# Optimization experiments

Measured on AMD Instinct MI355X. Metric: run time of the kernel, lower is better.

The kernel has to match this reference:

```python
import jax, jax.numpy as jnp
import numpy as np

NCH, P, T, BS = 129, 4, 64000, 8
FRM_RATE, TC, HAIR_TC, SHFT, FAC = 16, 8.0, 0.5, 0, 1.0
L_FRM = FRM_RATE * (2 ** (4 + SHFT))            # 256 samples per frame
ALPHA = float(np.exp(-1.0 / (TC * 2 ** (4 + SHFT))))       # temporal integrator pole
BETA = float(np.exp(-1.0 / (HAIR_TC * 2 ** (4 + SHFT))))   # hair-cell LPF pole


def setup_inputs() -> dict:
    rng = np.random.default_rng(0)
    # stable order-4 cochlear IIRs: 2 conjugate pole pairs inside unit circle
    r = rng.uniform(0.8, 0.97, (NCH, P // 2))
    th = rng.uniform(0.05, np.pi - 0.05, (NCH, P // 2))
    A = np.stack([
        np.poly(np.concatenate([r[c] * np.exp(1j * th[c]), r[c] * np.exp(-1j * th[c])])).real
        for c in range(NCH)
    ]).astype(np.float32)                        # [NCH, P+1], A[:,0]==1
    B = (rng.standard_normal((NCH, P + 1)) * 0.1).astype(np.float32)
    key = jax.random.key(0)
    wav = jax.random.normal(key, (BS, T), dtype=jnp.float32)
    return {"wavData": wav, "coch_B": jnp.asarray(B), "coch_A": jnp.asarray(A)}


def iir_lfilter(b, a, x):
    # b, a: [nCh, P+1] (a[:,0] == 1), x: [bs, T] -> y: [nCh, bs, T]
    # direct-form II transposed, all channels in one scan over time
    bt = b[:, None, :]                           # [nCh, 1, P+1]
    at = a[:, None, :]
    z0 = jnp.zeros((b.shape[0], x.shape[0], b.shape[1] - 1), x.dtype)

    def step(z, xt):                             # z: [nCh, bs, P], xt: [bs]
        y = bt[..., 0] * xt[None, :] + z[..., 0]
        z_shift = jnp.concatenate([z[..., 1:], jnp.zeros_like(z[..., :1])], -1)
        z = z_shift + bt[..., 1:] * xt[None, :, None] - at[..., 1:] * y[..., None]
        return z, y

    _, y = jax.lax.scan(step, z0, x.T)           # y: [T, nCh, bs]
    return jnp.moveaxis(y, 0, -1)                # [nCh, bs, T]


def first_order_iir(x, c):
    # y[t] = x[t] + c * y[t-1] along the last axis (lfilter b=[1,0], a=[1,-c])
    def combine(e1, e2):
        a1, b1 = e1
        a2, b2 = e2
        return a1 * a2, b1 * a2 + b2

    coef = jnp.full_like(x, jnp.asarray(c, x.dtype))
    _, y = jax.lax.associative_scan(combine, (coef, x), axis=-1)
    return y


def reference(wavData, coch_B, coch_A):
    y1 = iir_lfilter(coch_B, coch_A, wavData)        # cochlear filterbank [nCh, bs, T]
    y2 = jax.nn.sigmoid(FAC * y1)                    # hair-cell nonlinearity
    y2 = first_order_iir(y2, BETA)                   # hair-cell membrane LPF
    y2_prev = jnp.concatenate([y2[:1], y2[:-1]], 0)  # previous channel (ch 0 diffs itself -> 0)
    y4 = jnp.maximum(y2 - y2_prev, 0.0)              # lateral inhibition + half-wave rectify
    y5 = first_order_iir(y4, ALPHA)                  # temporal integration (alpha != 0 branch)
    aud = y5[..., 0:T - 1:L_FRM]                     # frame-rate downsample [nCh, bs, nFrm]
    return jnp.transpose(aud, (1, 0, 2))             # [bs, nCh, nFrm]
```

## Files before the change

### kernel.cpp

```cpp
#include <hip/hip_runtime.h>
#include <math.h>

#define NCH 129
#define BS 8
#define TLEN 64000
#define TILE 256
#define WARM 64
#define ZLEAD 256
#define NFRM 250
#define NSEQ (NCH * BS)
#define NBK (BS * NFRM)
#define KF_EDGE 8
#define KF_MAIN (NBK / 4)
#define MAXSEG 144

typedef float f2 __attribute__((ext_vector_type(2)));

__device__ __forceinline__ f2 mk2(float a, float b) { f2 r; r.x = a; r.y = b; return r; }

__device__ __forceinline__ f2 fma2(f2 a, f2 b, f2 c) {
#if __has_builtin(__builtin_elementwise_fma)
    return __builtin_elementwise_fma(a, b, c);
#else
    f2 r; r.x = fmaf(a.x, b.x, c.x); r.y = fmaf(a.y, b.y, c.y); return r;
#endif
}

__device__ __forceinline__ float sigf(float v) {
    return __builtin_amdgcn_rcpf(1.0f + __expf(-v));
}
__device__ __forceinline__ f2 sig2(f2 v) {
    f2 r; r.x = sigf(v.x); r.y = sigf(v.y); return r;
}

struct C2 { f2 b0, b1, b2, b3, b4, a1, a2, a3, a4; };

__device__ __forceinline__ C2 load_coef2(const float* __restrict__ B,
                                         const float* __restrict__ A,
                                         int cx, int cy) {
    C2 q;
    q.b0 = mk2(B[cx * 5 + 0], B[cy * 5 + 0]);
    q.b1 = mk2(B[cx * 5 + 1], B[cy * 5 + 1]);
    q.b2 = mk2(B[cx * 5 + 2], B[cy * 5 + 2]);
    q.b3 = mk2(B[cx * 5 + 3], B[cy * 5 + 3]);
    q.b4 = mk2(B[cx * 5 + 4], B[cy * 5 + 4]);
    q.a1 = mk2(A[cx * 5 + 1], A[cy * 5 + 1]);
    q.a2 = mk2(A[cx * 5 + 2], A[cy * 5 + 2]);
    q.a3 = mk2(A[cx * 5 + 3], A[cy * 5 + 3]);
    q.a4 = mk2(A[cx * 5 + 4], A[cy * 5 + 4]);
    return q;
}

__device__ __forceinline__ f2 iir2_step(const C2& q, float x,
                                        f2& z0, f2& z1, f2& z2, f2& z3) {
    f2 xx = mk2(x, x);
    f2 y = fma2(q.b0, xx, z0);
    z0 = fma2(-q.a1, y, fma2(q.b1, xx, z1));
    z1 = fma2(-q.a2, y, fma2(q.b2, xx, z2));
    z2 = fma2(-q.a3, y, fma2(q.b3, xx, z3));
    z3 = fma2(-q.a4, y, q.b4 * xx);
    return y;
}

#define ISTEP(xv) { (void)iir2_step(q, (xv), z0, z1, z2, z3); }
#define WSTEP(xv)                                                              \
    { f2 y_ = iir2_step(q, (xv), z0, z1, z2, z3);                              \
      u = fma2(beta2, u, sig2(y_)); }
#define MSTEP(xv)                                                              \
    { f2 y_ = iir2_step(q, (xv), z0, z1, z2, z3);                              \
      u = fma2(beta2, u, sig2(y_));                                            \
      float un_ = __shfl_down(u.x, 1, 64);                                     \
      float y4o_ = fmaxf(u.y - u.x, 0.0f);                                     \
      float y4e_ = fmaxf(pend_un - pend_ub, 0.0f);                             \
      g2 = fma2(alpha2, g2, mk2(y4o_, y4e_));                                  \
      pend_un = un_; pend_ub = u.y; }

__global__ __launch_bounds__(256, 8) void kF_fused(
        const float* __restrict__ wav, const float* __restrict__ B,
        const float* __restrict__ A, float* __restrict__ G,
        float* __restrict__ y4f, float beta, float alpha) {
    __shared__ float4 xs4[4 * MAXSEG];
    int blk = blockIdx.x;
    const f2 beta2 = mk2(beta, beta);
    const f2 alpha2 = mk2(alpha, alpha);

    if (blk < KF_EDGE) {
        int item = blk * 256 + threadIdx.x;
        if (item >= NBK) return;
        int b = item / NFRM;
        int r = item - b * NFRM;
        C2 q = load_coef2(B, A, 127, 128);
        f2 z0 = mk2(0.f, 0.f), z1 = z0, z2 = z0, z3 = z0, u = z0;
        int nIst = (r == 0) ? 0 : (r == 1 ? ZLEAD - WARM : ZLEAD);
        int nW   = (r == 0) ? 0 : WARM;
        const float* xg = wav + (size_t)b * TLEN
                        + (size_t)r * TILE - (size_t)(nIst + nW);
        #pragma unroll 2
        for (int j = 0; j < nIst; ++j) ISTEP(xg[j]);
        xg += nIst;
        #pragma unroll 2
        for (int j = 0; j < nW; ++j) WSTEP(xg[j]);
        xg += nW;
        float g4 = 0.f, yfirst = 0.f;
        #pragma unroll 2
        for (int j = 0; j < TILE; ++j) {
            f2 y_ = iir2_step(q, xg[j], z0, z1, z2, z3);
            u = fma2(beta2, u, sig2(y_));
            float y4 = fmaxf(u.y - u.x, 0.0f);
            if (j == 0) yfirst = y4;
            g4 = fmaf(alpha, g4, y4);
        }
        size_t idx = ((size_t)b * NFRM + r) * NCH + 128;
        G[idx] = g4;
        y4f[idx] = yfirst;
        return;
    }

    int wave = threadIdx.x >> 6;
    int t = threadIdx.x & 63;
    int tile = (blk - KF_EDGE) * 4 + wave;
    int b = tile / NFRM;
    int r = tile - b * NFRM;
    int gi = (r == 0) ? 0 : (r == 1 ? (ZLEAD - WARM) / 4 : ZLEAD / 4);
    int gw = (r == 0) ? 0 : WARM / 4;
    int gbase = gi + gw;
    int n4 = gbase + TILE / 4;
    const float* xg = wav + (size_t)b * TLEN
                    + (size_t)r * TILE - (size_t)(4 * gbase);
    float4* seg = xs4 + wave * MAXSEG;
    for (int i = t; i < n4; i += 64) seg[i] = ((const float4*)xg)[i];
    __syncthreads();

    int cA = 2 * t, cB = 2 * t + 1;
    C2 q = load_coef2(B, A, cA, cB);
    f2 z0 = mk2(0.f, 0.f), z1 = z0, z2 = z0, z3 = z0, u = z0;
    for (int g = 0; g < gi; ++g) {
        float4 xq = seg[g];
        ISTEP(xq.x); ISTEP(xq.y); ISTEP(xq.z); ISTEP(xq.w);
    }
    for (int g = gi; g < gbase; ++g) {
        float4 xq = seg[g];
        WSTEP(xq.x); WSTEP(xq.y); WSTEP(xq.z); WSTEP(xq.w);
    }

    f2 g2;
    float fo, fe, pend_un, pend_ub;
    {
        float4 xq = seg[gbase];
        f2 y_ = iir2_step(q, xq.x, z0, z1, z2, z3);
        u = fma2(beta2, u, sig2(y_));
        float un_ = __shfl_down(u.x, 1, 64);
        float y4o_ = fmaxf(u.y - u.x, 0.0f);
        fo = y4o_;
        g2 = mk2(y4o_, 0.0f);
        pend_un = un_; pend_ub = u.y;
        y_ = iir2_step(q, xq.y, z0, z1, z2, z3);
        u = fma2(beta2, u, sig2(y_));
        un_ = __shfl_down(u.x, 1, 64);
        y4o_ = fmaxf(u.y - u.x, 0.0f);
        float y4e_ = fmaxf(pend_un - pend_ub, 0.0f);
        fe = y4e_;
        g2 = fma2(alpha2, g2, mk2(y4o_, y4e_));
        pend_un = un_; pend_ub = u.y;
        MSTEP(xq.z); MSTEP(xq.w);
    }
    for (int g = gbase + 1; g < gbase + TILE / 4; ++g) {
        float4 xq = seg[g];
        MSTEP(xq.x); MSTEP(xq.y); MSTEP(xq.z); MSTEP(xq.w);
    }
    float y4e_last = fmaxf(pend_un - pend_ub, 0.0f);
    float go = g2.x;
    float ge = fmaf(alpha, g2.y, y4e_last);

    size_t base = ((size_t)b * NFRM + r) * NCH;
    G[base + cB] = go;
    y4f[base + cB] = fo;
    if (t < 63) {
        G[base + cB + 1] = ge;
        y4f[base + cB + 1] = fe;
    }
}

#define KD_LOAD(gn, yn, i)                                                     \
    {   int kk = k0 + (i); int kcl = (kk < NFRM) ? kk : (NFRM - 1);            \
        size_t ix = ((size_t)b * NFRM + kcl) * NCH + c;                        \
        gn = G[ix]; yn = y4f[ix];                                              \
        if (kk >= NFRM) { gn = 0.f; yn = 0.f; } }
#define KD_REPLAY(gn, yn, i)                                                   \
    {   int kk = k0 + (i);                                                     \
        if (kk < NFRM) o[kk] = fmaf(alpha, sv, yn);                            \
        sv = fmaf(aL, sv, gn); }

__global__ __launch_bounds__(256) void kD_scan_par(
        const float* __restrict__ G, const float* __restrict__ y4f,
        float* __restrict__ out, float alpha, float aL) {
    int id = blockIdx.x * 4 + (threadIdx.x >> 6);
    int lane = threadIdx.x & 63;
    if (id >= NSEQ) return;
    int b = id / NCH;
    int c = id - b * NCH;
    float* o = out + (size_t)id * NFRM;
    int k0 = lane * 4;
    if (c == 0) {
        #pragma unroll
        for (int i = 0; i < 4; ++i) {
            int kk = k0 + i;
            if (kk < NFRM) o[kk] = 0.0f;
        }
        return;
    }
    float g0, g1, g2v, g3, y0, y1, y2v, y3;
    KD_LOAD(g0, y0, 0); KD_LOAD(g1, y1, 1); KD_LOAD(g2v, y2v, 2); KD_LOAD(g3, y3, 3);
    float e = g0;
    e = fmaf(aL, e, g1);
    e = fmaf(aL, e, g2v);
    e = fmaf(aL, e, g3);
    float aL2 = aL * aL;
    float f = aL2 * aL2;
    for (int s = 0; s < 6; ++s) {
        int off = 1 << s;
        float src = __shfl_up(e, off, 64);
        if (lane < off) src = 0.f;
        e = fmaf(f, src, e);
        f = f * f;
    }
    float sv = __shfl_up(e, 1, 64);
    if (lane == 0) sv = 0.f;
    KD_REPLAY(g0, y0, 0); KD_REPLAY(g1, y1, 1);
    KD_REPLAY(g2v, y2v, 2); KD_REPLAY(g3, y3, 3);
}

extern "C" void kernel_launch(void* const* d_in, const int* in_sizes, int n_in,
                              void* d_out, int out_size, void* d_ws, size_t ws_size,
                              hipStream_t stream) {
    const float* wav = (const float*)d_in[0];
    const float* Bc  = (const float*)d_in[1];
    const float* Ac  = (const float*)d_in[2];
    float* out = (float*)d_out;

    float* G   = (float*)d_ws;
    float* y4f = G + (size_t)NBK * NCH;

    const float alpha  = (float)exp(-1.0 / 128.0);
    const float beta   = (float)exp(-1.0 / 8.0);
    const float alphaL = (float)exp(-256.0 / 128.0);

    kF_fused<<<KF_EDGE + KF_MAIN, 256, 0, stream>>>(wav, Bc, Ac, G, y4f, beta, alpha);
    kD_scan_par<<<NSEQ / 4, 256, 0, stream>>>(G, y4f, out, alpha, alphaL);
}
```

Before: 122.0 us.

## Shorten IIR warmup lead and replace parallel frame scan with sequential per-channel scan

Cuts the recomputed lead-in per tile from 256 to 192 IIR samples (plus the same 64 warm samples), which shrinks the shared segment buffer and reduces redundant filter work in the main kernel. The frame-level second pass changes from a 64-lane shuffle scan over 1032 waves to 8 blocks in which each thread walks one channel sequentially across 250 frames. The shorter lead trades some accuracy margin for less recomputation, since the filter state must decay within fewer samples. The sequential scan has very few waves and a 250-step dependent chain per thread, which may expose latency.

```diff
diff --git a/kernel.cpp b/kernel.cpp
--- a/kernel.cpp
+++ b/kernel.cpp
@@ -6,13 +6,15 @@
 #define TLEN 64000
 #define TILE 256
 #define WARM 64
-#define ZLEAD 256
 #define NFRM 250
 #define NSEQ (NCH * BS)
 #define NBK (BS * NFRM)
 #define KF_EDGE 8
 #define KF_MAIN (NBK / 4)
-#define MAXSEG 144
+#define GI 48
+#define GW 16
+#define GMAIN 64
+#define MAXSEG 128
 
 typedef float f2 __attribute__((ext_vector_type(2)));
 
@@ -91,8 +93,8 @@
         int r = item - b * NFRM;
         C2 q = load_coef2(B, A, 127, 128);
         f2 z0 = mk2(0.f, 0.f), z1 = z0, z2 = z0, z3 = z0, u = z0;
-        int nIst = (r == 0) ? 0 : (r == 1 ? ZLEAD - WARM : ZLEAD);
-        int nW   = (r == 0) ? 0 : WARM;
+        int nIst = (r == 0) ? 0 : 4 * GI;
+        int nW   = (r == 0) ? 0 : 4 * GW;
         const float* xg = wav + (size_t)b * TLEN
                         + (size_t)r * TILE - (size_t)(nIst + nW);
         #pragma unroll 2
@@ -121,10 +123,10 @@
     int tile = (blk - KF_EDGE) * 4 + wave;
     int b = tile / NFRM;
     int r = tile - b * NFRM;
-    int gi = (r == 0) ? 0 : (r == 1 ? (ZLEAD - WARM) / 4 : ZLEAD / 4);
-    int gw = (r == 0) ? 0 : WARM / 4;
+    int gi = (r == 0) ? 0 : GI;
+    int gw = (r == 0) ? 0 : GW;
     int gbase = gi + gw;
-    int n4 = gbase + TILE / 4;
+    int n4 = gbase + GMAIN;
     const float* xg = wav + (size_t)b * TLEN
                     + (size_t)r * TILE - (size_t)(4 * gbase);
     float4* seg = xs4 + wave * MAXSEG;
@@ -164,7 +166,7 @@
         pend_un = un_; pend_ub = u.y;
         MSTEP(xq.z); MSTEP(xq.w);
     }
-    for (int g = gbase + 1; g < gbase + TILE / 4; ++g) {
+    for (int g = gbase + 1; g < gbase + GMAIN; ++g) {
         float4 xq = seg[g];
         MSTEP(xq.x); MSTEP(xq.y); MSTEP(xq.z); MSTEP(xq.w);
     }
@@ -181,53 +183,32 @@
     }
 }
 
-#define KD_LOAD(gn, yn, i)                                                     \
-    {   int kk = k0 + (i); int kcl = (kk < NFRM) ? kk : (NFRM - 1);            \
-        size_t ix = ((size_t)b * NFRM + kcl) * NCH + c;                        \
-        gn = G[ix]; yn = y4f[ix];                                              \
-        if (kk >= NFRM) { gn = 0.f; yn = 0.f; } }
-#define KD_REPLAY(gn, yn, i)                                                   \
-    {   int kk = k0 + (i);                                                     \
-        if (kk < NFRM) o[kk] = fmaf(alpha, sv, yn);                            \
-        sv = fmaf(aL, sv, gn); }
-
-__global__ __launch_bounds__(256) void kD_scan_par(
+__global__ __launch_bounds__(256) void kD_scan_seq(
         const float* __restrict__ G, const float* __restrict__ y4f,
         float* __restrict__ out, float alpha, float aL) {
-    int id = blockIdx.x * 4 + (threadIdx.x >> 6);
-    int lane = threadIdx.x & 63;
-    if (id >= NSEQ) return;
-    int b = id / NCH;
-    int c = id - b * NCH;
-    float* o = out + (size_t)id * NFRM;
-    int k0 = lane * 4;
+    int b = blockIdx.x;
+    int c = threadIdx.x;
+    if (c > 128) return;
+    float* o = out + ((size_t)b * NCH + c) * NFRM;
     if (c == 0) {
-        #pragma unroll
-        for (int i = 0; i < 4; ++i) {
-            int kk = k0 + i;
-            if (kk < NFRM) o[kk] = 0.0f;
+        for (int k = 0; k < NFRM; ++k) o[k] = 0.0f;
+        return;
+    }
+    const float* gp = G + (size_t)b * NFRM * NCH + c;
+    const float* yp = y4f + (size_t)b * NFRM * NCH + c;
+    float s = 0.f;
+    float g = gp[0], y = yp[0];
+    #pragma unroll 2
+    for (int k = 0; k < NFRM; ++k) {
+        float gn = 0.f, yn = 0.f;
+        if (k + 1 < NFRM) {
+            gn = gp[(size_t)(k + 1) * NCH];
+            yn = yp[(size_t)(k + 1) * NCH];
         }
-        return;
-    }
-    float g0, g1, g2v, g3, y0, y1, y2v, y3;
-    KD_LOAD(g0, y0, 0); KD_LOAD(g1, y1, 1); KD_LOAD(g2v, y2v, 2); KD_LOAD(g3, y3, 3);
-    float e = g0;
-    e = fmaf(aL, e, g1);
-    e = fmaf(aL, e, g2v);
-    e = fmaf(aL, e, g3);
-    float aL2 = aL * aL;
-    float f = aL2 * aL2;
-    for (int s = 0; s < 6; ++s) {
-        int off = 1 << s;
-        float src = __shfl_up(e, off, 64);
-        if (lane < off) src = 0.f;
-        e = fmaf(f, src, e);
-        f = f * f;
-    }
-    float sv = __shfl_up(e, 1, 64);
-    if (lane == 0) sv = 0.f;
-    KD_REPLAY(g0, y0, 0); KD_REPLAY(g1, y1, 1);
-    KD_REPLAY(g2v, y2v, 2); KD_REPLAY(g3, y3, 3);
+        o[k] = fmaf(alpha, s, y);
+        s = fmaf(aL, s, g);
+        g = gn; y = yn;
+    }
 }
 
 extern "C" void kernel_launch(void* const* d_in, const int* in_sizes, int n_in,
@@ -246,5 +227,5 @@
     const float alphaL = (float)exp(-256.0 / 128.0);
 
     kF_fused<<<KF_EDGE + KF_MAIN, 256, 0, stream>>>(wav, Bc, Ac, G, y4f, beta, alpha);
-    kD_scan_par<<<NSEQ / 4, 256, 0, stream>>>(G, y4f, out, alpha, alphaL);
-}
+    kD_scan_seq<<<BS, 256, 0, stream>>>(G, y4f, out, alpha, alphaL);
+}
```

After: 166.8 us. 36.7% more time.
